# Performance work log

Hardware: AMD Instinct MI355X
Metric: run time of the kernel (lower is better)

Reference implementation:

```python
import jax, jax.numpy as jnp
import numpy as np

jax.config.update("jax_enable_x64", True)  # original torch code runs in float64; minors underflow fp32

D = 96   # Nsites
N = 48   # Nparticles


def setup_inputs() -> dict:
    key = jax.random.key(0)
    # Orthonormal single-particle orbitals (columns), as the module assumes (P^T P = I)
    A = jax.random.normal(key, (D, D), dtype=jnp.float64)
    Q, _ = jnp.linalg.qr(A)
    P = Q[:, :N]  # [D, N]
    # A valid ordered particle configuration: strictly increasing, occ_positions[k] <= D-N+k
    occ_positions = jnp.arange(N, dtype=jnp.int32) * (D // N)  # stride-2 filling
    return {"P": P, "occ_positions": occ_positions}


def _cond_probs(P, occ_positions):
    """Conditional probabilities probs[k, x] of placing the k-th (ordered) particle at
    site x given particles 0..k-1 at occ_positions[0..k-1].

    Math identical to SlaterDetSampler_ordered.get_cond_prob (naive_update=True):
      G = I - P P^T
      probs[k,x] = -det(M_x[0:x+1,0:x+1]) / det(M[0:xmin,0:xmin])
    where M = G - diag(occupancy of particles < k) and M_x additionally sets n_x = 1.
    Since Ksites is always the contiguous range 0..x, all determinants are LEADING
    principal minors; and because only the (x,x) diagonal entry changes by -1 (last index
    of the block), det(M_x block) = d_{x+1} - d_x with d_j the leading j-minor of M.
    """
    Dd, Nn = P.shape
    dt = P.dtype
    eye = jnp.eye(Dd, dtype=dt)
    G = eye - P @ P.T                                             # [D, D]

    onehots = jax.nn.one_hot(occ_positions, Dd, dtype=dt)         # [N, D]
    n_before = jnp.cumsum(onehots, axis=0) - onehots              # occupancy of particles < k
    A = G[None] - n_before[:, :, None] * eye                      # [N, D, D]: G - diag(n_<k)

    # All leading principal minors via batched det of masked matrices:
    # M_j = A on the [0:j,0:j] block, identity elsewhere  =>  det(M_j) = leading j-minor
    ii = jnp.arange(Dd)
    jj = jnp.arange(1, Dd + 1)
    blk = (ii[None, :, None] < jj[:, None, None]) & (ii[None, None, :] < jj[:, None, None])  # [D,D,D]
    Ms = jnp.where(blk[None], A[:, None], eye)                    # [N, D, D, D]
    d = jnp.linalg.det(Ms.reshape(Nn * Dd, Dd, Dd)).reshape(Nn, Dd)
    d_full = jnp.concatenate([jnp.ones((Nn, 1), dt), d], axis=1)  # d_full[k, j] = j-th leading minor

    k = jnp.arange(Nn)
    xmin = jnp.where(k == 0, 0, occ_positions[jnp.maximum(k - 1, 0)] + 1)  # [N]
    xmax = Dd - Nn + k + 1                                                  # [N]
    denom = jnp.take_along_axis(d_full, xmin[:, None], axis=1)              # [N, 1]
    num = d_full[:, 1:] - d_full[:, :-1]                                    # det(GG_num) per candidate x

    x = jnp.arange(Dd)
    support = (x[None, :] >= xmin[:, None]) & (x[None, :] < xmax[:, None])
    probs = jnp.where(support, -num / denom, jnp.zeros((), dt))
    # torch.where(abs(probs) > 1e-15, probs, 0.)
    probs = jnp.where(jnp.abs(probs) > 1e-15, probs, jnp.zeros((), dt))
    return probs


def reference(P, occ_positions):
    probs = _cond_probs(P, occ_positions)                          # [N, D]
    # prob of the full ordered sample = prod_k probs[k, occ_positions[k]]  (as in sample())
    p_k = jnp.take_along_axis(probs, occ_positions[:, None], axis=1)[:, 0]
    prob_sample = jnp.prod(p_k)
    return probs, prob_sample
```

## Files before the change

kernel.cpp:

```cpp
#include <hip/hip_runtime.h>
#include <math.h>

#define Dd 96
#define Nn 48
#define LD 97
#define PTS 98

__device__ __forceinline__ double frcp(double x) {
    double r = __builtin_amdgcn_rcp(x);
    r = fma(fma(-x, r, 1.0), r, r);
    r = fma(fma(-x, r, 1.0), r, r);
    return r;
}

__global__ __launch_bounds__(512, 1) void slater_kernel(const float* __restrict__ P,
                                                        const int* __restrict__ occ,
                                                        float* __restrict__ out,
                                                        unsigned* __restrict__ cnt) {
    __shared__ double As[Dd * LD];
    __shared__ unsigned char flag[Dd];
    float* PT = (float*)As;

    const int tid  = threadIdx.x;
    const int k    = blockIdx.x;
    const int n    = Dd - Nn + k + 1;
    const int lane = tid & 63;
    const int wave = tid >> 6;
    const int xmin = (k == 0) ? 0 : occ[k - 1] + 1;

    if (tid < Dd) flag[tid] = 0;
    __syncthreads();
    if (tid < k) flag[occ[tid]] = 1;
    for (int e = tid; e < Dd * Nn; e += 512) {
        int c = e / Nn, t = e - (e / Nn) * Nn;
        PT[t * PTS + c] = P[e];
    }
    __syncthreads();

    double Areg[12]; int trs[3], tcs[3];
#pragma unroll
    for (int it = 0; it < 3; ++it) {
        int tau = tid + 512 * it;
        double s00 = 0.0, s01 = 0.0, s10 = 0.0, s11 = 0.0;
        int tr = 0, tc = 0;
        if (tau < 1176) {
            tr = (int)((97.0 - sqrt(9409.0 - 8.0 * (double)tau)) * 0.5);
            while ((tr * (97 - tr)) / 2 > tau) --tr;
            while (((tr + 1) * (96 - tr)) / 2 <= tau) ++tr;
            tc = tr + (tau - (tr * (97 - tr)) / 2);
            int r0 = 2 * tr, c0 = 2 * tc;
            if (r0 < n && c0 < n) {
                for (int t = 0; t < Nn; ++t) {
                    const float* row = PT + t * PTS;
                    float2 pr = *(const float2*)(row + r0);
                    float2 pc = *(const float2*)(row + c0);
                    s00 -= (double)pr.x * (double)pc.x; s01 -= (double)pr.x * (double)pc.y;
                    s10 -= (double)pr.y * (double)pc.x; s11 -= (double)pr.y * (double)pc.y;
                }
            }
        }
        trs[it] = tr; tcs[it] = tc;
        Areg[it * 4 + 0] = s00; Areg[it * 4 + 1] = s01;
        Areg[it * 4 + 2] = s10; Areg[it * 4 + 3] = s11;
    }
    __syncthreads();
#pragma unroll
    for (int it = 0; it < 3; ++it) {
        int tau = tid + 512 * it;
        if (tau < 1176) {
            int tr = trs[it], tc = tcs[it];
            int r0 = 2 * tr, c0 = 2 * tc;
            if (r0 < n && c0 < n) {
                bool r1 = (r0 + 1 < n), c1 = (c0 + 1 < n);
                double d0 = flag[r0] ? 0.0 : 1.0;
                double d1 = flag[r0 + 1] ? 0.0 : 1.0;
                As[r0 * LD + c0] = Areg[it * 4 + 0] + ((r0 == c0) ? d0 : 0.0);
                if (c1)       As[r0 * LD + c0 + 1]       = Areg[it * 4 + 1];
                if (r1)       As[(r0 + 1) * LD + c0]     = Areg[it * 4 + 2];
                if (r1 && c1) As[(r0 + 1) * LD + c0 + 1] = Areg[it * 4 + 3] + ((r0 == c0) ? d1 : 0.0);
                if (tr != tc) {
                    As[c0 * LD + r0] = Areg[it * 4 + 0];
                    if (c1)       As[(c0 + 1) * LD + r0]     = Areg[it * 4 + 1];
                    if (r1)       As[c0 * LD + r0 + 1]       = Areg[it * 4 + 2];
                    if (r1 && c1) As[(c0 + 1) * LD + r0 + 1] = Areg[it * 4 + 3];
                }
            }
        }
    }
    __syncthreads();

    double runprod = 1.0;
    double myprob  = 0.0;
    bool   dead    = false;

    auto guard = [&](int jj, double pivot) {
        double ap = fabs(pivot);
        if (jj >= xmin) {
            if (tid == jj) myprob = runprod * (1.0 - pivot);
            double newrun = runprod * pivot;
            if (!(ap > 1e-7) || !(ap < 8.0) || !(fabs(newrun) > 1e-8)) dead = true;
            else runprod = newrun;
        } else {
            if (!(ap > 1e-12) || !(ap < 8.0)) dead = true;
        }
    };

    int j = 0;
    for (; !dead && j + 4 <= n - 1; j += 4) {
        int t = n - (j + 4);
        bool ok0 = (lane < t), ok1 = (lane + 64 < t);
        int c0 = j + 4 + (ok0 ? lane : 0);
        int c1 = j + 4 + (ok1 ? lane + 64 : 0);
        double R0c0 = As[j * LD + c0],       R1c0 = As[(j + 1) * LD + c0];
        double R2c0 = As[(j + 2) * LD + c0], R3c0 = As[(j + 3) * LD + c0];
        double R0c1 = As[j * LD + c1],       R1c1 = As[(j + 1) * LD + c1];
        double R2c1 = As[(j + 2) * LD + c1], R3c1 = As[(j + 3) * LD + c1];

        const double* Bp0 = As + j * LD + j;
        const double* Bp1 = Bp0 + LD;
        const double* Bp2 = Bp1 + LD;
        const double* Bp3 = Bp2 + LD;
        double B00 = Bp0[0], B01 = Bp0[1], B02 = Bp0[2], B03 = Bp0[3];
        double B10 = Bp1[0], B11 = Bp1[1], B12 = Bp1[2], B13 = Bp1[3];
        double B20 = Bp2[0], B21 = Bp2[1], B22 = Bp2[2], B23 = Bp2[3];
        double B30 = Bp3[0], B31 = Bp3[1], B32 = Bp3[2], B33 = Bp3[3];

        double piv0 = B00;
        double rp0  = frcp(piv0);
        double m10  = B10 * rp0;
        double u01 = B01, u02 = B02, u03 = B03;
        double piv1 = B11 - m10 * u01;
        double u12  = B12 - m10 * u02;
        double u13  = B13 - m10 * u03;
        double rp1  = frcp(piv1);
        double m20  = B20 * rp0;
        double m21  = (B21 - m20 * u01) * rp1;
        double piv2 = B22 - m20 * u02 - m21 * u12;
        double u23  = B23 - m20 * u03 - m21 * u13;
        double rp2  = frcp(piv2);
        double m30  = B30 * rp0;
        double m31  = (B31 - m30 * u01) * rp1;
        double m32  = (B32 - m30 * u02 - m31 * u12) * rp2;
        double piv3 = B33 - m30 * u03 - m31 * u13 - m32 * u23;
        double rp3  = frcp(piv3);

        guard(j + 0, piv0);
        if (!dead) guard(j + 1, piv1);
        if (!dead) guard(j + 2, piv2);
        if (!dead) guard(j + 3, piv3);

        if (!dead) {
            for (int i = j + 4 + wave; i < n; i += 32) {
                double a0[4], a1[4], a2[4], a3[4], T0[4], T1[4];
                bool h[4];
#pragma unroll
                for (int u = 0; u < 4; ++u) {
                    int r = i + u * 8;
                    h[u] = (r < n);
                    const double* rw = As + (h[u] ? r : i) * LD;
                    a0[u] = rw[j];     a1[u] = rw[j + 1];
                    a2[u] = rw[j + 2]; a3[u] = rw[j + 3];
                    T0[u] = rw[c0];    T1[u] = rw[c1];
                }
#pragma unroll
                for (int u = 0; u < 4; ++u) {
                    double m0 = a0[u] * rp0;
                    double m1 = (a1[u] - m0 * u01) * rp1;
                    double m2 = (a2[u] - m0 * u02 - m1 * u12) * rp2;
                    double m3 = (a3[u] - m0 * u03 - m1 * u13 - m2 * u23) * rp3;
                    double w3 = m3;
                    double w2 = m2 - m32 * w3;
                    double w1 = m1 - m21 * w2 - m31 * w3;
                    double w0 = m0 - m10 * w1 - m20 * w2 - m30 * w3;
                    if (h[u]) {
                        double* rw = As + (i + u * 8) * LD;
                        if (ok0) rw[c0] = T0[u] - w0 * R0c0 - w1 * R1c0 - w2 * R2c0 - w3 * R3c0;
                        if (ok1) rw[c1] = T1[u] - w0 * R0c1 - w1 * R1c1 - w2 * R2c1 - w3 * R3c1;
                    }
                }
            }
        }
        __syncthreads();
    }

    for (; !dead && j < n - 1; ++j) {
        double pivot = As[j * LD + j];
        guard(j, pivot);
        if (dead) break;
        double rp = frcp(pivot);
        int t = n - 1 - j;
        double r0 = (lane < t)      ? As[j * LD + j + 1 + lane]  : 0.0;
        double r1 = (lane + 64 < t) ? As[j * LD + j + 65 + lane] : 0.0;
        for (int i = j + 1 + wave; i < n; i += 8) {
            double mult = As[i * LD + j] * rp;
            if (lane < t)      As[i * LD + j + 1 + lane]  -= mult * r0;
            if (lane + 64 < t) As[i * LD + j + 65 + lane] -= mult * r1;
        }
        __syncthreads();
    }
    if (!dead && tid == n - 1) {
        double pl = As[(n - 1) * LD + (n - 1)];
        myprob = runprod * (1.0 - pl);
    }

    if (tid < Dd) {
        double p = myprob;
        if (!isfinite(p)) p = 0.0;
        if (!(fabs(p) > 1e-15)) p = 0.0;
        p = fmin(fmax(p, 0.0), 1.0);
        out[k * Dd + tid] = (float)p;
    }

    __threadfence();
    __syncthreads();
    if (wave == 0) {
        int old = 0;
        if (lane == 0)
            old = (int)__hip_atomic_fetch_add(cnt, 1u, __ATOMIC_ACQ_REL,
                                              __HIP_MEMORY_SCOPE_AGENT);
        old = __shfl(old, 0, 64);
        if (((unsigned)old + 1u) % (unsigned)Nn == 0u) {
            __threadfence();
            double v = 1.0;
            if (lane < Nn) {
                float f = __hip_atomic_load(out + lane * Dd + occ[lane],
                                            __ATOMIC_RELAXED, __HIP_MEMORY_SCOPE_AGENT);
                v = (double)f;
            }
#pragma unroll
            for (int off = 32; off >= 1; off >>= 1)
                v *= __shfl_down(v, off, 64);
            if (lane == 0) {
                if (!isfinite(v)) v = 0.0;
                out[Nn * Dd] = (float)v;
            }
        }
    }
}

extern "C" void kernel_launch(void* const* d_in, const int* in_sizes, int n_in,
                              void* d_out, int out_size, void* d_ws, size_t ws_size,
                              hipStream_t stream) {
    const float* P = (const float*)d_in[0];
    const int* occ = (const int*)d_in[1];
    float* out = (float*)d_out;

    slater_kernel<<<Nn, 512, 0, stream>>>(P, occ, out, (unsigned*)d_ws);
}
```

Measured before the change: 108.3 us.

## Double block size to 1024 threads and precompute per-column Schur solve

Raises the workgroup size from 512 to 1024 threads and rescales all strided loops and row interleaving to match. In the blocked LU trailing update, the 4x4 triangular solve against the two target columns is now done once per step per thread instead of once per row. Each row update then reduces to a dot product of the row's four panel entries with the precomputed coefficients. This cuts per-row FP64 work, but the larger block risks register pressure and adds synchronization cost on a single block.

```diff
diff --git a/kernel.cpp b/kernel.cpp
--- a/kernel.cpp
+++ b/kernel.cpp
@@ -13,10 +13,10 @@
     return r;
 }
 
-__global__ __launch_bounds__(512, 1) void slater_kernel(const float* __restrict__ P,
-                                                        const int* __restrict__ occ,
-                                                        float* __restrict__ out,
-                                                        unsigned* __restrict__ cnt) {
+__global__ __launch_bounds__(1024, 1) void slater_kernel(const float* __restrict__ P,
+                                                         const int* __restrict__ occ,
+                                                         float* __restrict__ out,
+                                                         unsigned* __restrict__ cnt) {
     __shared__ double As[Dd * LD];
     __shared__ unsigned char flag[Dd];
     float* PT = (float*)As;
@@ -31,16 +31,16 @@
     if (tid < Dd) flag[tid] = 0;
     __syncthreads();
     if (tid < k) flag[occ[tid]] = 1;
-    for (int e = tid; e < Dd * Nn; e += 512) {
+    for (int e = tid; e < Dd * Nn; e += 1024) {
         int c = e / Nn, t = e - (e / Nn) * Nn;
         PT[t * PTS + c] = P[e];
     }
     __syncthreads();
 
-    double Areg[12]; int trs[3], tcs[3];
-#pragma unroll
-    for (int it = 0; it < 3; ++it) {
-        int tau = tid + 512 * it;
+    double Areg[8]; int trs[2], tcs[2];
+#pragma unroll
+    for (int it = 0; it < 2; ++it) {
+        int tau = tid + 1024 * it;
         double s00 = 0.0, s01 = 0.0, s10 = 0.0, s11 = 0.0;
         int tr = 0, tc = 0;
         if (tau < 1176) {
@@ -65,8 +65,8 @@
     }
     __syncthreads();
 #pragma unroll
-    for (int it = 0; it < 3; ++it) {
-        int tau = tid + 512 * it;
+    for (int it = 0; it < 2; ++it) {
+        int tau = tid + 1024 * it;
         if (tau < 1176) {
             int tr = trs[it], tc = tcs[it];
             int r0 = 2 * tr, c0 = 2 * tc;
@@ -150,12 +150,29 @@
         if (!dead) guard(j + 3, piv3);
 
         if (!dead) {
-            for (int i = j + 4 + wave; i < n; i += 32) {
+            double y0 = R0c0;
+            double y1 = R1c0 - m10 * y0;
+            double y2 = R2c0 - m20 * y0 - m21 * y1;
+            double y3 = R3c0 - m30 * y0 - m31 * y1 - m32 * y2;
+            double s3c0 = y3 * rp3;
+            double s2c0 = (y2 - u23 * s3c0) * rp2;
+            double s1c0 = (y1 - u12 * s2c0 - u13 * s3c0) * rp1;
+            double s0c0 = (y0 - u01 * s1c0 - u02 * s2c0 - u03 * s3c0) * rp0;
+            double z0 = R0c1;
+            double z1 = R1c1 - m10 * z0;
+            double z2 = R2c1 - m20 * z0 - m21 * z1;
+            double z3 = R3c1 - m30 * z0 - m31 * z1 - m32 * z2;
+            double s3c1 = z3 * rp3;
+            double s2c1 = (z2 - u23 * s3c1) * rp2;
+            double s1c1 = (z1 - u12 * s2c1 - u13 * s3c1) * rp1;
+            double s0c1 = (z0 - u01 * s1c1 - u02 * s2c1 - u03 * s3c1) * rp0;
+
+            for (int i = j + 4 + wave; i < n; i += 64) {
                 double a0[4], a1[4], a2[4], a3[4], T0[4], T1[4];
                 bool h[4];
 #pragma unroll
                 for (int u = 0; u < 4; ++u) {
-                    int r = i + u * 8;
+                    int r = i + u * 16;
                     h[u] = (r < n);
                     const double* rw = As + (h[u] ? r : i) * LD;
                     a0[u] = rw[j];     a1[u] = rw[j + 1];
@@ -164,18 +181,12 @@
                 }
 #pragma unroll
                 for (int u = 0; u < 4; ++u) {
-                    double m0 = a0[u] * rp0;
-                    double m1 = (a1[u] - m0 * u01) * rp1;
-                    double m2 = (a2[u] - m0 * u02 - m1 * u12) * rp2;
-                    double m3 = (a3[u] - m0 * u03 - m1 * u13 - m2 * u23) * rp3;
-                    double w3 = m3;
-                    double w2 = m2 - m32 * w3;
-                    double w1 = m1 - m21 * w2 - m31 * w3;
-                    double w0 = m0 - m10 * w1 - m20 * w2 - m30 * w3;
                     if (h[u]) {
-                        double* rw = As + (i + u * 8) * LD;
-                        if (ok0) rw[c0] = T0[u] - w0 * R0c0 - w1 * R1c0 - w2 * R2c0 - w3 * R3c0;
-                        if (ok1) rw[c1] = T1[u] - w0 * R0c1 - w1 * R1c1 - w2 * R2c1 - w3 * R3c1;
+                        double* rw = As + (i + u * 16) * LD;
+                        if (ok0) rw[c0] = T0[u] - a0[u] * s0c0 - a1[u] * s1c0
+                                                - a2[u] * s2c0 - a3[u] * s3c0;
+                        if (ok1) rw[c1] = T1[u] - a0[u] * s0c1 - a1[u] * s1c1
+                                                - a2[u] * s2c1 - a3[u] * s3c1;
                     }
                 }
             }
@@ -191,7 +202,7 @@
         int t = n - 1 - j;
         double r0 = (lane < t)      ? As[j * LD + j + 1 + lane]  : 0.0;
         double r1 = (lane + 64 < t) ? As[j * LD + j + 65 + lane] : 0.0;
-        for (int i = j + 1 + wave; i < n; i += 8) {
+        for (int i = j + 1 + wave; i < n; i += 16) {
             double mult = As[i * LD + j] * rp;
             if (lane < t)      As[i * LD + j + 1 + lane]  -= mult * r0;
             if (lane + 64 < t) As[i * LD + j + 65 + lane] -= mult * r1;
@@ -245,5 +256,5 @@
     const int* occ = (const int*)d_in[1];
     float* out = (float*)d_out;
 
-    slater_kernel<<<Nn, 512, 0, stream>>>(P, occ, out, (unsigned*)d_ws);
+    slater_kernel<<<Nn, 1024, 0, stream>>>(P, occ, out, (unsigned*)d_ws);
 }
```

Measured after the change: 109.2 us. Within noise of the previous version (+0.9%).
